# Kernel tuning notes

Hardware: AMD Instinct MI355X
Metric: run time of the kernel (lower is better)

The kernel has to match this reference:

```python
import jax, jax.numpy as jnp
import numpy as np

N = 50000      # nodes
E = 800000     # edges
F_IN = 128     # input features
H = 8          # heads
F = 16         # features per head
NEG_SLOPE = 0.2


def setup_inputs() -> dict:
    key = jax.random.key(0)
    k_x, k_ei, k_w, k_as, k_ad = jax.random.split(key, 5)
    x = jax.random.normal(k_x, (N, F_IN), dtype=jnp.float32)
    edge_index = jax.random.randint(k_ei, (2, E), 0, N, dtype=jnp.int64)
    # learned params (PyG GATConv: lin weight [H*F, F_in] no bias; att_src/att_dst [H, F]; out bias [H*F])
    glorot = lambda k, shp: jax.random.uniform(k, shp, jnp.float32, -1.0, 1.0) * np.sqrt(6.0 / (shp[-1] + shp[-2]))
    W = glorot(k_w, (H * F, F_IN))
    att_src = glorot(k_as, (H, F))
    att_dst = glorot(k_ad, (H, F))
    bias = jnp.zeros((H * F,), dtype=jnp.float32)  # bias_init = zeros_
    return {"x": x, "W": W, "att_src": att_src, "att_dst": att_dst, "bias": bias, "edge_index": edge_index}


def reference(x, W, att_src, att_dst, bias, edge_index):
    # linear projection, split heads: [N, H, F]
    h = (x @ W.T).reshape(N, H, F)
    # per-node attention logits: [N, H]
    a_src = jnp.einsum('nhf,hf->nh', h, att_src)
    a_dst = jnp.einsum('nhf,hf->nh', h, att_dst)
    src, dst = edge_index[0], edge_index[1]
    # edge scores + LeakyReLU: [E, H]
    e = a_src[src] + a_dst[dst]
    e = jnp.where(e >= 0, e, NEG_SLOPE * e)
    # segment softmax over incoming edges of each dst node
    m = jax.ops.segment_max(e, dst, num_segments=N)          # [N, H]
    ex = jnp.exp(e - m[dst])                                  # [E, H]
    denom = jax.ops.segment_sum(ex, dst, num_segments=N)     # [N, H]
    alpha = ex / (denom[dst] + 1e-16)                         # [E, H]
    # weighted scatter-aggregate of source features
    msg = alpha[:, :, None] * h[src]                          # [E, H, F]
    out = jax.ops.segment_sum(msg, dst, num_segments=N)      # [N, H, F]
    return out.reshape(N, H * F) + bias
```

## Files before the change

### kernel.cpp

```cpp
#include <hip/hip_runtime.h>

#define NEG_SLOPE 0.2f
#define HEADS 8
#define FEAT 16
#define HF 128
#define FIN 128
#define BROWS 64
#define PITCH 136
#define BSHIFT 5
#define BNODES 32
#define NBUCKMAX 1600
#define CHUNK 3200
#define NSBMAX 256
#define SCAP 16
#define CAP 1024
#define CSTRIDE 256

typedef __bf16 bf16x8 __attribute__((ext_vector_type(8)));
typedef float  f32x4  __attribute__((ext_vector_type(4)));

__device__ __forceinline__ bool detect_i64(const int* ei) {
    return (ei[1] | ei[3] | ei[5] | ei[7]) == 0;
}
__device__ __forceinline__ int load_idx(const int* ei, long long pos, bool is64) {
    return is64 ? ei[2 * pos] : ei[pos];
}

__device__ __forceinline__ float bf2f(unsigned u) { return __uint_as_float(u << 16); }

__device__ __forceinline__ unsigned short f2bf(float f) {
    unsigned u = __float_as_uint(f);
    unsigned r = u + 0x7fffu + ((u >> 16) & 1u);
    return (unsigned short)(r >> 16);
}

__global__ __launch_bounds__(1024) void binsort_kernel(
    const int* __restrict__ ei, unsigned* __restrict__ ebuf,
    int* __restrict__ cnt2, int E, int nb, int nsb)
{
    __shared__ int lh[NBUCKMAX];
    const int t = threadIdx.x;
    const int blk = blockIdx.x;
    const bool is64 = detect_i64(ei);
    const int e0 = blk * CHUNK;

    for (int b = t; b < nb; b += 1024) lh[b] = 0;
    __syncthreads();

#pragma unroll
    for (int i = 0; i < 4; ++i) {
        const int r = i * 1024 + t;
        if (r < CHUNK) {
            const int e = e0 + r;
            if (e < E) {
                const unsigned s = (unsigned)load_idx(ei, e, is64);
                const unsigned d = (unsigned)load_idx(ei, (long long)E + e, is64);
                const int bkt = (int)(d >> BSHIFT);
                const int ofs = atomicAdd(&lh[bkt], 1);
                if (ofs < SCAP)
                    ebuf[((size_t)bkt * nsb + blk) * SCAP + ofs] = s | (d << 16);
            }
        }
    }
    __syncthreads();
    for (int b = t; b < nb; b += 1024)
        cnt2[(size_t)b * CSTRIDE + blk] = min(lh[b], SCAP);
}

__global__ __launch_bounds__(256) void proj_kernel(
    const float* __restrict__ x, const float* __restrict__ W,
    const float* __restrict__ att_src, const float* __restrict__ att_dst,
    unsigned short* __restrict__ hb, float* __restrict__ a_src,
    float* __restrict__ a_dst, int N)
{
    __shared__ __align__(16) unsigned short xs[(BROWS + FIN) * PITCH];
    unsigned short* wsl = xs + BROWS * PITCH;
    const int t = threadIdx.x;
    const int n0 = blockIdx.x * BROWS;

#pragma unroll
    for (int i = 0; i < 8; ++i) {
        const int f4 = i * 256 + t;
        const int r = f4 >> 5, c4 = f4 & 31;
        const int rr = (n0 + r < N) ? (n0 + r) : (N - 1);
        const float4 v = ((const float4*)(x + (size_t)rr * FIN))[c4];
        unsigned short* p = &xs[r * PITCH + c4 * 4];
        p[0] = f2bf(v.x); p[1] = f2bf(v.y); p[2] = f2bf(v.z); p[3] = f2bf(v.w);
    }
#pragma unroll
    for (int i = 0; i < 16; ++i) {
        const int f4 = i * 256 + t;
        const int r = f4 >> 5, c4 = f4 & 31;
        const float4 v = ((const float4*)(W + (size_t)r * FIN))[c4];
        unsigned short* p = &wsl[r * PITCH + c4 * 4];
        p[0] = f2bf(v.x); p[1] = f2bf(v.y); p[2] = f2bf(v.z); p[3] = f2bf(v.w);
    }
    __syncthreads();

    const int w = t >> 6, lane = t & 63;
    const int lrow = lane & 15;
    const int lk = lane >> 4;
    const int r0 = w * 16;

    f32x4 acc[8];
#pragma unroll
    for (int i = 0; i < 8; ++i) { f32x4 z = {0.f, 0.f, 0.f, 0.f}; acc[i] = z; }

#pragma unroll
    for (int ks = 0; ks < 4; ++ks) {
        const int kb = ks * 32 + lk * 8;
        const bf16x8 af = *(const bf16x8*)&xs[(r0 + lrow) * PITCH + kb];
#pragma unroll
        for (int tt = 0; tt < 8; ++tt) {
            const bf16x8 bf = *(const bf16x8*)&wsl[(tt * 16 + lrow) * PITCH + kb];
            acc[tt] = __builtin_amdgcn_mfma_f32_16x16x32_bf16(af, bf, acc[tt], 0, 0, 0);
        }
    }
    __syncthreads();

#pragma unroll
    for (int tt = 0; tt < 8; ++tt) {
#pragma unroll
        for (int rg = 0; rg < 4; ++rg) {
            const int row = r0 + lk * 4 + rg;
            const int col = tt * 16 + lrow;
            xs[row * PITCH + col] = f2bf(acc[tt][rg]);
        }
    }
    __syncthreads();

#pragma unroll
    for (int i = 0; i < 8; ++i) {
        const int u4 = i * 256 + t;
        const int r = u4 >> 5, c4 = u4 & 31;
        if (n0 + r < N) {
            const unsigned short* p = &xs[r * PITCH + c4 * 4];
            ushort4 v; v.x = p[0]; v.y = p[1]; v.z = p[2]; v.w = p[3];
            ((ushort4*)hb)[(size_t)(n0 + r) * (HF / 4) + c4] = v;
        }
    }
#pragma unroll
    for (int i = 0; i < 2; ++i) {
        const int p = i * 256 + t;
        const int r = p >> 3, hd = p & 7;
        if (n0 + r < N) {
            float s = 0.f, d = 0.f;
#pragma unroll
            for (int j = 0; j < FEAT; ++j) {
                const float hv = bf2f(xs[r * PITCH + hd * FEAT + j]);
                s = fmaf(hv, att_src[hd * FEAT + j], s);
                d = fmaf(hv, att_dst[hd * FEAT + j], d);
            }
            a_src[(size_t)(n0 + r) * HEADS + hd] = s;
            a_dst[(size_t)(n0 + r) * HEADS + hd] = d;
        }
    }
}

__global__ __launch_bounds__(256) void bucket_agg(
    const unsigned* __restrict__ ebuf, const int* __restrict__ cnt2,
    const float* __restrict__ a_src, const float* __restrict__ a_dst,
    const unsigned short* __restrict__ hb, const float* __restrict__ bias,
    float* __restrict__ out, int N, int nsb)
{
    __shared__ unsigned up[NSBMAX * SCAP];
    __shared__ unsigned srt[CAP];
    __shared__ int scnt[256];
    __shared__ int cnts[BNODES], sc[BNODES], cur[BNODES];
    const int b = blockIdx.x;
    const int t = threadIdx.x;
    const int w = t >> 6, lane = t & 63;
    const int nw = nsb * SCAP;

    scnt[t] = (t < nsb) ? cnt2[(size_t)b * CSTRIDE + t] : 0;
    if (t < BNODES) cnts[t] = 0;
    for (int j = t; j < nw; j += 256)
        up[j] = ebuf[(size_t)b * nw + j];
    __syncthreads();

    for (int j = t; j < nw; j += 256)
        if ((j & (SCAP - 1)) < scnt[j >> 4])
            atomicAdd(&cnts[(up[j] >> 16) & (BNODES - 1)], 1);
    __syncthreads();

    if (t < BNODES) {
        const int c = cnts[t];
        int sx = c;
#pragma unroll
        for (int off = 1; off < BNODES; off <<= 1) {
            const int y = __shfl_up(sx, off, 64);
            if (t >= off) sx += y;
        }
        sc[t] = sx;
        cur[t] = sx - c;
    }
    __syncthreads();

    for (int j = t; j < nw; j += 256)
        if ((j & (SCAP - 1)) < scnt[j >> 4]) {
            const unsigned p = up[j];
            const int dl = (p >> 16) & (BNODES - 1);
            const int ofs = atomicAdd(&cur[dl], 1);
            if (ofs < CAP) srt[ofs] = p & 0xffffu;
        }
    __syncthreads();

    const int hd  = lane >> 3;
    const int h_w = lane & 7;
    const int ew  = lane >> 3;
    const float2 b2 = ((const float2*)bias)[lane];

#pragma unroll 1
    for (int i = 0; i < BNODES / 4; ++i) {
        const int dl = w * (BNODES / 4) + i;
        const int d = b * BNODES + dl;
        if (d >= N) break;
        const int end = min(sc[dl], CAP);
        const int beg = max(end - cnts[dl], 0);
        const float adh_w = a_dst[d * HEADS + h_w];

        float acc0 = 0.f, acc1 = 0.f, den = 0.f;
        for (int j = beg; j < end; j += 8) {
            unsigned p[8]; float wg[8];
#pragma unroll
            for (int k = 0; k < 8; ++k) {
                const int s = (int)srt[min(j + k, end - 1)];
                p[k] = *(const unsigned*)(hb + (size_t)s * HF + 2 * lane);
            }
            const int sw = (int)srt[min(j + ew, end - 1)];
            float vv = a_src[sw * HEADS + h_w] + adh_w;
            vv = vv >= 0.f ? vv : NEG_SLOPE * vv;
            const float wv = __expf(vv);
#pragma unroll
            for (int k = 0; k < 8; ++k) {
                const float g = __shfl(wv, (k << 3) | hd, 64);
                wg[k] = (j + k < end) ? g : 0.f;
            }
#pragma unroll
            for (int k = 0; k < 8; ++k) {
                acc0 = fmaf(wg[k], bf2f(p[k] & 0xffffu), acc0);
                acc1 = fmaf(wg[k], bf2f(p[k] >> 16),     acc1);
                den += wg[k];
            }
        }
        const float inv = 1.f / (den + 1e-16f);
        float2 o2;
        o2.x = fmaf(acc0, inv, b2.x);
        o2.y = fmaf(acc1, inv, b2.y);
        ((float2*)out)[(size_t)d * (HF / 2) + lane] = o2;
    }
}

extern "C" void kernel_launch(void* const* d_in, const int* in_sizes, int n_in,
                              void* d_out, int out_size, void* d_ws, size_t ws_size,
                              hipStream_t stream)
{
    const float* x       = (const float*)d_in[0];
    const float* W       = (const float*)d_in[1];
    const float* att_src = (const float*)d_in[2];
    const float* att_dst = (const float*)d_in[3];
    const float* bias    = (const float*)d_in[4];
    const int*   ei      = (const int*)d_in[5];
    float* out = (float*)d_out;

    const int N = in_sizes[0] / FIN;
    const int E = in_sizes[5] / 2;
    const int NBUCK = (N + BNODES - 1) >> BSHIFT;
    const int NSB = (E + CHUNK - 1) / CHUNK;
    const int PB = (N + BROWS - 1) / BROWS;

    char* ws = (char*)d_ws;
    unsigned short* hb = (unsigned short*)ws; ws += (size_t)N * HF * 2;
    unsigned* ebuf = (unsigned*)ws; ws += (size_t)NBUCK * NSB * SCAP * 4;
    int* cnt2      = (int*)ws;  ws += (size_t)NBUCK * CSTRIDE * sizeof(int);
    float* a_src  = (float*)ws; ws += (size_t)N * HEADS * sizeof(float);
    float* a_dst  = (float*)ws; ws += (size_t)N * HEADS * sizeof(float);

    hipLaunchKernelGGL(binsort_kernel, dim3(NSB), dim3(1024), 0, stream,
                       ei, ebuf, cnt2, E, NBUCK, NSB);
    hipLaunchKernelGGL(proj_kernel, dim3(PB), dim3(256), 0, stream,
                       x, W, att_src, att_dst, hb, a_src, a_dst, N);
    hipLaunchKernelGGL(bucket_agg, dim3(NBUCK), dim3(256), 0, stream,
                       ebuf, cnt2, a_src, a_dst, hb, bias, out, N, NSB);
}
```

Before: 157.1 us.

## Precompute per-edge attention weights into shared memory before aggregation

Adds a block-wide pass that computes exp(leakyrelu(a_src+a_dst)) for every edge in the bucket with vectorized a_src loads, storing the results in LDS that is aliased over the staging buffer. The aggregation loop then reads the weights from shared memory instead of doing per-iteration gathers, exp and cross-lane shuffles. The padded min-clamped tail is replaced by exact 8/4/1 remainder loops. a_dst for the block's nodes is also staged into shared memory. The cost is an extra sync and a larger LDS footprint (32KB for the weights), which may lower occupancy.

Measured after the change: 164.1 us. +4.5%, slower.

```diff
diff --git a/kernel.cpp b/kernel.cpp
--- a/kernel.cpp
+++ b/kernel.cpp
@@ -163,10 +163,12 @@
     const unsigned short* __restrict__ hb, const float* __restrict__ bias,
     float* __restrict__ out, int N, int nsb)
 {
-    __shared__ unsigned up[NSBMAX * SCAP];
+    __shared__ __align__(16) float wf[CAP * HEADS];
     __shared__ unsigned srt[CAP];
     __shared__ int scnt[256];
+    __shared__ float adl[BNODES * HEADS];
     __shared__ int cnts[BNODES], sc[BNODES], cur[BNODES];
+    unsigned* up = (unsigned*)wf;
     const int b = blockIdx.x;
     const int t = threadIdx.x;
     const int w = t >> 6, lane = t & 63;
@@ -174,6 +176,10 @@
 
     scnt[t] = (t < nsb) ? cnt2[(size_t)b * CSTRIDE + t] : 0;
     if (t < BNODES) cnts[t] = 0;
+    {
+        const int g = b * (BNODES * HEADS) + t;
+        adl[t] = (g < N * HEADS) ? a_dst[g] : 0.f;
+    }
     for (int j = t; j < nw; j += 256)
         up[j] = ebuf[(size_t)b * nw + j];
     __syncthreads();
@@ -201,13 +207,36 @@
             const unsigned p = up[j];
             const int dl = (p >> 16) & (BNODES - 1);
             const int ofs = atomicAdd(&cur[dl], 1);
-            if (ofs < CAP) srt[ofs] = p & 0xffffu;
-        }
-    __syncthreads();
-
-    const int hd  = lane >> 3;
-    const int h_w = lane & 7;
-    const int ew  = lane >> 3;
+            if (ofs < CAP) srt[ofs] = (unsigned)(dl << 16) | (p & 0xffffu);
+        }
+    __syncthreads();
+
+    const int cntb = min(sc[BNODES - 1], CAP);
+    for (int j = t; j < cntb; j += 256) {
+        const unsigned e = srt[j];
+        const int s = (int)(e & 0xffffu);
+        const int dl = (int)(e >> 16);
+        const float4 a0 = ((const float4*)(a_src + (size_t)s * HEADS))[0];
+        const float4 a1 = ((const float4*)(a_src + (size_t)s * HEADS))[1];
+        float v[8];
+        v[0] = a0.x + adl[dl * HEADS + 0]; v[1] = a0.y + adl[dl * HEADS + 1];
+        v[2] = a0.z + adl[dl * HEADS + 2]; v[3] = a0.w + adl[dl * HEADS + 3];
+        v[4] = a1.x + adl[dl * HEADS + 4]; v[5] = a1.y + adl[dl * HEADS + 5];
+        v[6] = a1.z + adl[dl * HEADS + 6]; v[7] = a1.w + adl[dl * HEADS + 7];
+        float4 w0, w1;
+#pragma unroll
+        for (int h = 0; h < 8; ++h) {
+            float vv = v[h] >= 0.f ? v[h] : NEG_SLOPE * v[h];
+            v[h] = __expf(vv);
+        }
+        w0.x = v[0]; w0.y = v[1]; w0.z = v[2]; w0.w = v[3];
+        w1.x = v[4]; w1.y = v[5]; w1.z = v[6]; w1.w = v[7];
+        ((float4*)&wf[j * HEADS])[0] = w0;
+        ((float4*)&wf[j * HEADS])[1] = w1;
+    }
+    __syncthreads();
+
+    const int hd = lane >> 3;
     const float2 b2 = ((const float2*)bias)[lane];
 
 #pragma unroll 1
@@ -217,31 +246,48 @@
         if (d >= N) break;
         const int end = min(sc[dl], CAP);
         const int beg = max(end - cnts[dl], 0);
-        const float adh_w = a_dst[d * HEADS + h_w];
 
         float acc0 = 0.f, acc1 = 0.f, den = 0.f;
-        for (int j = beg; j < end; j += 8) {
+        int j = beg;
+        for (; j + 8 <= end; j += 8) {
             unsigned p[8]; float wg[8];
 #pragma unroll
             for (int k = 0; k < 8; ++k) {
-                const int s = (int)srt[min(j + k, end - 1)];
+                const int s = (int)(srt[j + k] & 0xffffu);
                 p[k] = *(const unsigned*)(hb + (size_t)s * HF + 2 * lane);
             }
-            const int sw = (int)srt[min(j + ew, end - 1)];
-            float vv = a_src[sw * HEADS + h_w] + adh_w;
-            vv = vv >= 0.f ? vv : NEG_SLOPE * vv;
-            const float wv = __expf(vv);
-#pragma unroll
-            for (int k = 0; k < 8; ++k) {
-                const float g = __shfl(wv, (k << 3) | hd, 64);
-                wg[k] = (j + k < end) ? g : 0.f;
-            }
+#pragma unroll
+            for (int k = 0; k < 8; ++k) wg[k] = wf[(j + k) * HEADS + hd];
 #pragma unroll
             for (int k = 0; k < 8; ++k) {
                 acc0 = fmaf(wg[k], bf2f(p[k] & 0xffffu), acc0);
                 acc1 = fmaf(wg[k], bf2f(p[k] >> 16),     acc1);
                 den += wg[k];
             }
+        }
+        for (; j + 4 <= end; j += 4) {
+            unsigned p[4]; float wg[4];
+#pragma unroll
+            for (int k = 0; k < 4; ++k) {
+                const int s = (int)(srt[j + k] & 0xffffu);
+                p[k] = *(const unsigned*)(hb + (size_t)s * HF + 2 * lane);
+            }
+#pragma unroll
+            for (int k = 0; k < 4; ++k) wg[k] = wf[(j + k) * HEADS + hd];
+#pragma unroll
+            for (int k = 0; k < 4; ++k) {
+                acc0 = fmaf(wg[k], bf2f(p[k] & 0xffffu), acc0);
+                acc1 = fmaf(wg[k], bf2f(p[k] >> 16),     acc1);
+                den += wg[k];
+            }
+        }
+        for (; j < end; ++j) {
+            const int s = (int)(srt[j] & 0xffffu);
+            const unsigned p = *(const unsigned*)(hb + (size_t)s * HF + 2 * lane);
+            const float wg = wf[j * HEADS + hd];
+            acc0 = fmaf(wg, bf2f(p & 0xffffu), acc0);
+            acc1 = fmaf(wg, bf2f(p >> 16), acc1);
+            den += wg;
         }
         const float inv = 1.f / (den + 1e-16f);
         float2 o2;
```
